# Kernel optimization log

Hardware: AMD Instinct MI355X
Metric: run time of the kernel (lower is better)

## Reference

```python
import jax, jax.numpy as jnp
import numpy as np

N = 64  # num_nodes


def setup_inputs() -> dict:
    key = jax.random.key(0)
    k1, k2, k3, k4 = jax.random.split(key, 4)
    x = jax.random.normal(k1, (N, N), dtype=jnp.float32)
    weights_t = jax.random.normal(k2, (N, N), dtype=jnp.float32)
    weights_r = jax.random.normal(k3, (N, N, N, N), dtype=jnp.float32)
    # r_zeros = 0 and column-stochastic r_const guarantee each per-(s,t)
    # predecessor matrix has eigenvalue exactly 1 (as assumed by torch.eig
    # selection in the original RBC code).
    r_zeros = jnp.zeros((N, N, N, N), dtype=jnp.float32)
    rc = jax.random.uniform(k4, (N, N, N, N), dtype=jnp.float32, minval=0.05, maxval=1.0)
    r_const = rc / jnp.sum(rc, axis=2, keepdims=True)  # columns (axis -2) sum to 1
    return {"x": x, "weights_t": weights_t, "weights_r": weights_r,
            "r_zeros": r_zeros, "r_const": r_const}


def _eigvec_at_one(M):
    # M: (..., n, n) real. Batched nonsymmetric eig; pick eigenvalue closest
    # to 1+0j (robust equivalent of the original exact match to [1., 0.]),
    # return its (real) right eigenvector.
    n = M.shape[-1]
    w, vr = jnp.linalg.eig(M.reshape(-1, n, n))          # (B, n), (B, n, n) complex
    idx = jnp.argmin(jnp.abs(w - 1.0), axis=-1)          # (B,)
    v = jnp.take_along_axis(vr, idx[:, None, None], axis=-1)[..., 0].real  # (B, n)
    return v.reshape(M.shape[:-2] + (n,))


def reference(x, weights_t, weights_r, r_zeros, r_const):
    n = x.shape[0]
    i = jnp.arange(n)
    # layer2[s,t,s,s] = x[s,t] * W_t[s,t] * r_const[s,t,s,s]
    r_diag = r_const[i[:, None], i[None, :], i[:, None], i[:, None]]  # (n, n)
    T = x * weights_t * r_diag                                        # (n, n)
    # predecessor prob matrices (detached in the original)
    M = jax.lax.stop_gradient(weights_r * r_zeros + r_const)          # (n, n, n, n)
    v = _eigvec_at_one(M)                                             # (n, n, n) = (s, t, node)
    denom = v[i[:, None], i[None, :], i[:, None]]                     # v[s, t, s]
    # sum over all (s,t) of T[s,t]/v[s,t,s] * v[s,t,:]
    rbc = jnp.einsum('st,stn->n', T / denom, v)
    return rbc
```

## Files before the change

### kernel.cpp

```cpp
#include <hip/hip_runtime.h>

#define NN 64
#define NITER 20

__global__ __launch_bounds__(64, 4) void perron_kernel(
    const float* __restrict__ x,
    const float* __restrict__ wt,
    const float* __restrict__ rconst,
    float* __restrict__ ws)
{
    const int st = blockIdx.x;
    const int m  = threadIdx.x;
    const int s  = st >> 6;

    const float* M = rconst + (size_t)st * (NN * NN);

    float4 row[16];
    const float4* M4 = (const float4*)(M + m * NN);
    #pragma unroll
    for (int q = 0; q < 16; ++q) row[q] = M4[q];

    __shared__ float vbuf[2][NN];
    vbuf[0][m] = 1.0f / NN;
    __syncthreads();

    int cur = 0;
    for (int it = 0; it < NITER; ++it) {
        const float4* v4 = (const float4*)vbuf[cur];
        float acc = 0.0f;
        #pragma unroll
        for (int q = 0; q < 16; ++q) {
            float4 v = v4[q];
            acc += row[q].x * v.x;
            acc += row[q].y * v.y;
            acc += row[q].z * v.z;
            acc += row[q].w * v.w;
        }
        cur ^= 1;
        vbuf[cur][m] = acc;
        __syncthreads();
    }

    const float Mss  = M[s * NN + s];
    const float coef = x[st] * wt[st] * Mss / vbuf[cur][s];
    ws[(size_t)st * NN + m] = coef * vbuf[cur][m];
}

__global__ __launch_bounds__(256) void reduce_kernel(
    const float* __restrict__ ws, float* __restrict__ out)
{
    const int n   = blockIdx.x;
    const int tid = threadIdx.x;
    float acc = 0.0f;
    #pragma unroll
    for (int r = 0; r < 16; ++r)
        acc += ws[(size_t)(tid + 256 * r) * NN + n];

    #pragma unroll
    for (int off = 32; off > 0; off >>= 1)
        acc += __shfl_down(acc, off, 64);

    __shared__ float wsum[4];
    if ((tid & 63) == 0) wsum[tid >> 6] = acc;
    __syncthreads();
    if (tid == 0) out[n] = wsum[0] + wsum[1] + wsum[2] + wsum[3];
}

extern "C" void kernel_launch(void* const* d_in, const int* in_sizes, int n_in,
                              void* d_out, int out_size, void* d_ws, size_t ws_size,
                              hipStream_t stream) {
    const float* x      = (const float*)d_in[0];
    const float* wt     = (const float*)d_in[1];
    const float* rconst = (const float*)d_in[4];
    float* out = (float*)d_out;
    float* ws  = (float*)d_ws;

    perron_kernel<<<dim3(NN * NN), dim3(NN), 0, stream>>>(x, wt, rconst, ws);
    reduce_kernel<<<dim3(NN), dim3(256), 0, stream>>>(ws, out);
}
```

Baseline: 176.6 us.

## Replace LDS power-iteration exchange with readlane broadcasts and cut iteration count

The power-iteration vector no longer goes through shared memory with a barrier each step. Each lane keeps its component in a register and the other lanes read it with readlane broadcasts. The first iteration is folded into the row load as a row-sum, and the total iteration count drops from 20 to 11. Four independent accumulators shorten the dependency chain. The main risk is accuracy, since fewer power iterations may not converge well enough for matrices whose second eigenvalue is not small.

```diff
diff --git a/kernel.cpp b/kernel.cpp
--- a/kernel.cpp
+++ b/kernel.cpp
@@ -1,7 +1,11 @@
 #include <hip/hip_runtime.h>
 
 #define NN 64
-#define NITER 20
+#define NITER 11
+
+__device__ __forceinline__ float bcast_lane(float v, int lane) {
+    return __uint_as_float(__builtin_amdgcn_readlane(__float_as_uint(v), lane));
+}
 
 __global__ __launch_bounds__(64, 4) void perron_kernel(
     const float* __restrict__ x,
@@ -15,35 +19,33 @@
 
     const float* M = rconst + (size_t)st * (NN * NN);
 
-    float4 row[16];
+    float4 row4[16];
     const float4* M4 = (const float4*)(M + m * NN);
+    float acc = 0.0f;
     #pragma unroll
-    for (int q = 0; q < 16; ++q) row[q] = M4[q];
+    for (int q = 0; q < 16; ++q) {
+        row4[q] = M4[q];
+        acc += (row4[q].x + row4[q].y) + (row4[q].z + row4[q].w);
+    }
+    acc *= (1.0f / NN);
 
-    __shared__ float vbuf[2][NN];
-    vbuf[0][m] = 1.0f / NN;
-    __syncthreads();
-
-    int cur = 0;
     for (int it = 0; it < NITER; ++it) {
-        const float4* v4 = (const float4*)vbuf[cur];
-        float acc = 0.0f;
+        const float v = acc;
+        float a0 = 0.f, a1 = 0.f, a2 = 0.f, a3 = 0.f;
         #pragma unroll
         for (int q = 0; q < 16; ++q) {
-            float4 v = v4[q];
-            acc += row[q].x * v.x;
-            acc += row[q].y * v.y;
-            acc += row[q].z * v.z;
-            acc += row[q].w * v.w;
+            a0 += row4[q].x * bcast_lane(v, 4 * q + 0);
+            a1 += row4[q].y * bcast_lane(v, 4 * q + 1);
+            a2 += row4[q].z * bcast_lane(v, 4 * q + 2);
+            a3 += row4[q].w * bcast_lane(v, 4 * q + 3);
         }
-        cur ^= 1;
-        vbuf[cur][m] = acc;
-        __syncthreads();
+        acc = (a0 + a1) + (a2 + a3);
     }
 
+    const float vs   = bcast_lane(acc, s);
     const float Mss  = M[s * NN + s];
-    const float coef = x[st] * wt[st] * Mss / vbuf[cur][s];
-    ws[(size_t)st * NN + m] = coef * vbuf[cur][m];
+    const float coef = x[st] * wt[st] * Mss / vs;
+    ws[(size_t)st * NN + m] = coef * acc;
 }
 
 __global__ __launch_bounds__(256) void reduce_kernel(
```

New measurement: 175.6 us. Within noise of the previous version (-0.5%).
